# Performance work log

Measured on AMD Instinct MI355X. Metric: run time of the kernel, lower is better.

Reference implementation:

```python
import jax, jax.numpy as jnp
import numpy as np

HID, NBINS = 256, 4
NMIR, NMRNA, B, NP, PD = 2000, 20000, 16, 2048, 1024
EREG, EPM, EPI = 300000, 320000, 32000


def _lin(x, w, b):
    return x @ w.T + b


def _gelu(x):
    # torch nn.GELU default = exact erf formulation
    return jax.nn.gelu(x, approximate=False)


def _ln(x, g, b):
    m = jnp.mean(x, axis=-1, keepdims=True)
    v = jnp.mean((x - m) ** 2, axis=-1, keepdims=True)
    return (x - m) * jax.lax.rsqrt(v + 1e-5) * g + b


def setup_inputs() -> dict:
    key = jax.random.key(0)
    ks = jax.random.split(key, 48)

    def lin_w(i, dout, din):
        s = 1.0 / np.sqrt(din)
        return jax.random.uniform(ks[i], (dout, din), minval=-s, maxval=s, dtype=jnp.float32)

    inp = {}
    inp['emb_mirna'] = jax.random.normal(ks[0], (NMIR, HID), jnp.float32) * 0.02
    inp['emb_mrna'] = jax.random.normal(ks[1], (NMRNA, HID), jnp.float32) * 0.02
    inp['w_mir2mrna'] = jax.random.uniform(ks[2], (EREG,), jnp.float32)
    inp['w_mrna2mir'] = jax.random.uniform(ks[3], (EREG,), jnp.float32)
    inp['w_mrna2pat'] = jax.random.uniform(ks[4], (EPM,), jnp.float32)
    inp['w_mir2pat'] = jax.random.uniform(ks[5], (EPI,), jnp.float32)
    inp['reg_w_mrna'] = lin_w(6, HID, HID)
    inp['reg_b_mrna'] = jnp.zeros((HID,), jnp.float32)
    inp['reg_w_mirna'] = lin_w(7, HID, HID)
    inp['reg_b_mirna'] = jnp.zeros((HID,), jnp.float32)
    inp['proj_w'] = lin_w(8, HID, HID)
    inp['proj_b'] = jnp.zeros((HID,), jnp.float32)
    inp['ln_g'] = jnp.ones((HID,), jnp.float32)
    inp['ln_b'] = jnp.zeros((HID,), jnp.float32)
    inp['omics_w'] = lin_w(9, NBINS, HID)
    inp['omics_b'] = jnp.zeros((NBINS,), jnp.float32)
    inp['wsi_w'] = lin_w(10, HID, PD)
    inp['wsi_b'] = jnp.zeros((HID,), jnp.float32)
    inp['mlp_w'] = lin_w(11, HID, HID)
    inp['mlp_b'] = jnp.zeros((HID,), jnp.float32)
    inp['wln_g'] = jnp.ones((HID,), jnp.float32)
    inp['wln_b'] = jnp.zeros((HID,), jnp.float32)
    inp['fuse_w1'] = lin_w(12, HID, 2 * HID)
    inp['fuse_b1'] = jnp.zeros((HID,), jnp.float32)
    inp['fuse_w2'] = lin_w(13, NBINS, HID)
    inp['fuse_b2'] = jnp.zeros((NBINS,), jnp.float32)
    inp['patches'] = jax.random.normal(ks[14], (B, NP, PD), jnp.float32)
    inp['mask'] = jnp.ones((B, NP), jnp.float32)
    inp['src_mir2mrna'] = jax.random.randint(ks[15], (EREG,), 0, NMIR, jnp.int32)
    inp['dst_mir2mrna'] = jax.random.randint(ks[16], (EREG,), 0, NMRNA, jnp.int32)
    inp['src_mrna2mir'] = jax.random.randint(ks[17], (EREG,), 0, NMRNA, jnp.int32)
    inp['dst_mrna2mir'] = jax.random.randint(ks[18], (EREG,), 0, NMIR, jnp.int32)
    inp['src_mrna2pat'] = jax.random.randint(ks[19], (EPM,), 0, NMRNA, jnp.int32)
    inp['dst_mrna2pat'] = jax.random.randint(ks[20], (EPM,), 0, B, jnp.int32)
    inp['src_mir2pat'] = jax.random.randint(ks[21], (EPI,), 0, NMIR, jnp.int32)
    inp['dst_mir2pat'] = jax.random.randint(ks[22], (EPI,), 0, B, jnp.int32)
    return inp


def reference(emb_mirna, emb_mrna, w_mir2mrna, w_mrna2mir, w_mrna2pat, w_mir2pat,
              reg_w_mrna, reg_b_mrna, reg_w_mirna, reg_b_mirna,
              proj_w, proj_b, ln_g, ln_b, omics_w, omics_b,
              wsi_w, wsi_b, mlp_w, mlp_b, wln_g, wln_b,
              fuse_w1, fuse_b1, fuse_w2, fuse_b2, patches, mask,
              src_mir2mrna, dst_mir2mrna, src_mrna2mir, dst_mrna2mir,
              src_mrna2pat, dst_mrna2pat, src_mir2pat, dst_mir2pat):
    # ---- omics: node embeddings (nid = arange -> full tables) ----
    h_mir, h_mrna = emb_mirna, emb_mrna
    # ---- SimpleRegEncoder: weighted gather-scatter-sum per etype (on ORIGINAL h) ----
    agg_mrna = jax.ops.segment_sum(h_mir[src_mir2mrna] * w_mir2mrna[:, None], dst_mir2mrna, num_segments=NMRNA)
    agg_mir = jax.ops.segment_sum(h_mrna[src_mrna2mir] * w_mrna2mir[:, None], dst_mrna2mir, num_segments=NMIR)
    h_mrna = h_mrna + _gelu(_lin(agg_mrna, reg_w_mrna, reg_b_mrna))  # dropout = identity (eval)
    h_mir = h_mir + _gelu(_lin(agg_mir, reg_w_mirna, reg_b_mirna))
    # ---- PatientReadout: cross_reducer='sum' over both gene->patient etypes ----
    acc = (jax.ops.segment_sum(h_mrna[src_mrna2pat] * w_mrna2pat[:, None], dst_mrna2pat, num_segments=B)
           + jax.ops.segment_sum(h_mir[src_mir2pat] * w_mir2pat[:, None], dst_mir2pat, num_segments=B))
    pat = _ln(_gelu(_lin(acc, proj_w, proj_b)), ln_g, ln_b)  # [B, HID]
    omics_logits = _lin(pat, omics_w, omics_b)  # [B, NBINS]
    # ---- SimpleWSIEncoder ----
    x = _lin(patches, wsi_w, wsi_b)  # [B, NP, HID]
    denom = jnp.clip(jnp.sum(mask, axis=1, keepdims=True), 1.0, None)
    pooled = jnp.sum(x * mask[:, :, None], axis=1) / denom
    pooled = _gelu(_lin(_gelu(pooled), mlp_w, mlp_b))
    wsi = _ln(pooled, wln_g, wln_b)  # [B, HID]
    # ---- fusion head ----
    cat = jnp.concatenate([pat, wsi], axis=-1)  # [B, 2*HID]
    fused = _lin(_gelu(_lin(cat, fuse_w1, fuse_b1)), fuse_w2, fuse_b2)  # [B, NBINS]
    return fused, omics_logits
```

## Files before the change

kernel.cpp:

```cpp
#include <hip/hip_runtime.h>
#include <math.h>

#define HID 256
#define NBINS 4
#define NMIR 2000
#define NMRNA 20000
#define NG (NMRNA + NMIR)
#define BB 16
#define NP 2048
#define PD 1024
#define EREG 300000
#define EPM 320000
#define EPI 32000

typedef __attribute__((ext_vector_type(8))) short bf16x8;
typedef __attribute__((ext_vector_type(4))) float f32x4;

__device__ __forceinline__ float gelu_exact(float x) {
    return 0.5f * x * (1.0f + erff(x * 0.7071067811865475f));
}

__device__ __forceinline__ unsigned short f2b(float f) {
    union { float f; unsigned int u; } v; v.f = f;
    unsigned int u = v.u + 0x7fffu + ((v.u >> 16) & 1u);
    return (unsigned short)(u >> 16);
}

__device__ __forceinline__ float block_reduce_sum(float v, float* red) {
    int c = threadIdx.x;
    red[c] = v;
    __syncthreads();
    for (int st = 128; st > 0; st >>= 1) {
        if (c < st) red[c] += red[c + st];
        __syncthreads();
    }
    float r = red[0];
    __syncthreads();
    return r;
}

__device__ __forceinline__ float kred(float v, float* red, int b, int kk) {
    red[kk * 16 + b] = v;
    __syncthreads();
    for (int st = 8; st >= 1; st >>= 1) {
        if (kk < st) red[kk * 16 + b] += red[(kk + st) * 16 + b];
        __syncthreads();
    }
    float r = red[b];
    __syncthreads();
    return r;
}

__global__ void k_f2b_w(const float* __restrict__ wA, const float* __restrict__ wB,
                        unsigned short* __restrict__ out) {
    int i = blockIdx.x * blockDim.x + threadIdx.x;
    if (i < HID * HID) out[i] = f2b(wA[i]);
    else if (i < 2 * HID * HID) out[i] = f2b(wB[i - HID * HID]);
}

__global__ void k_hist2(const int* __restrict__ dA, const int* __restrict__ dB,
                        int* __restrict__ cnt) {
    int i = blockIdx.x * blockDim.x + threadIdx.x;
    if (i < EREG) atomicAdd(&cnt[dA[i]], 1);
    else if (i < 2 * EREG) atomicAdd(&cnt[NMRNA + dB[i - EREG]], 1);
}

__global__ __launch_bounds__(1024) void k_scan2(const int* __restrict__ cnt,
                                                int* __restrict__ rpA, int* __restrict__ cuA,
                                                int* __restrict__ rpB, int* __restrict__ cuB) {
    __shared__ int part[1024];
    const int* c = (blockIdx.x == 0) ? cnt : cnt + NMRNA;
    int n = (blockIdx.x == 0) ? NMRNA : NMIR;
    int* rowptr = (blockIdx.x == 0) ? rpA : rpB;
    int* cursor = (blockIdx.x == 0) ? cuA : cuB;
    int t = threadIdx.x;
    int chunk = (n + 1023) >> 10;
    int beg = t * chunk;
    int end = min(beg + chunk, n);
    int s = 0;
    for (int i = beg; i < end; i++) s += c[i];
    part[t] = s;
    __syncthreads();
    for (int st = 1; st < 1024; st <<= 1) {
        int v = (t >= st) ? part[t - st] : 0;
        __syncthreads();
        part[t] += v;
        __syncthreads();
    }
    int off = part[t] - s;
    for (int i = beg; i < end; i++) {
        rowptr[i] = off;
        cursor[i] = off;
        off += c[i];
    }
    if (end == n) rowptr[n] = off;
}

__global__ void k_place2(
        const int* __restrict__ srcA, const int* __restrict__ dstA, const float* __restrict__ wA,
        int* __restrict__ cuA, int* __restrict__ srcpA, float* __restrict__ wpA,
        const int* __restrict__ srcB, const int* __restrict__ dstB, const float* __restrict__ wB,
        int* __restrict__ cuB, int* __restrict__ srcpB, float* __restrict__ wpB) {
    int i = blockIdx.x * blockDim.x + threadIdx.x;
    if (i < EREG) {
        int p = atomicAdd(&cuA[dstA[i]], 1);
        srcpA[p] = srcA[i];
        wpA[p] = wA[i];
    } else if (i < 2 * EREG) {
        int j = i - EREG;
        int p = atomicAdd(&cuB[dstB[j]], 1);
        srcpB[p] = srcB[j];
        wpB[p] = wB[j];
    }
}

__global__ __launch_bounds__(256) void k_gather2(
        const float* __restrict__ emb_mirna, const float* __restrict__ emb_mrna,
        const int* __restrict__ rpA, const int* __restrict__ srcpA, const float* __restrict__ wpA,
        const int* __restrict__ rpB, const int* __restrict__ srcpB, const float* __restrict__ wpB,
        unsigned short* __restrict__ agg) {
    __shared__ float lacc[4][HID];
    int n = blockIdx.x;
    const float* emb;
    const int* rp; const int* srcp; const float* wp;
    int node;
    if (n < NMRNA) { emb = emb_mirna; rp = rpA; srcp = srcpA; wp = wpA; node = n; }
    else           { emb = emb_mrna;  rp = rpB; srcp = srcpB; wp = wpB; node = n - NMRNA; }
    int wv = threadIdx.x >> 6, lane = threadIdx.x & 63;
    int beg = rp[node], end = rp[node + 1];
    float a0 = 0.f, a1 = 0.f, a2 = 0.f, a3 = 0.f;
    for (int j = beg + wv; j < end; j += 4) {
        int s = srcp[j];
        float we = wp[j];
        const float* hp = emb + (size_t)s * HID;
        a0 += we * hp[lane];
        a1 += we * hp[lane + 64];
        a2 += we * hp[lane + 128];
        a3 += we * hp[lane + 192];
    }
    lacc[wv][lane] = a0;
    lacc[wv][lane + 64] = a1;
    lacc[wv][lane + 128] = a2;
    lacc[wv][lane + 192] = a3;
    __syncthreads();
    int c = threadIdx.x;
    agg[(size_t)n * HID + c] = f2b(lacc[0][c] + lacc[1][c] + lacc[2][c] + lacc[3][c]);
}

__global__ __launch_bounds__(256) void k_update2(
        const unsigned short* __restrict__ A,
        const float* __restrict__ emb_mrna, const float* __restrict__ emb_mirna,
        const unsigned short* __restrict__ wb,
        const float* __restrict__ bias_mrna, const float* __restrict__ bias_mirna,
        float* __restrict__ h) {
    int row0 = blockIdx.x * 16;
    const float* emb; const unsigned short* Wb; const float* bias; int base;
    if (row0 < NMRNA) { emb = emb_mrna;  Wb = wb;             bias = bias_mrna;  base = 0; }
    else              { emb = emb_mirna; Wb = wb + HID * HID; bias = bias_mirna; base = NMRNA; }
    int wv = threadIdx.x >> 6;
    int lane = threadIdx.x & 63;
    int m = lane & 15;
    int q = lane >> 4;
    bf16x8 afrag[8];
    const unsigned short* arow = A + (size_t)(row0 + m) * HID + q * 8;
#pragma unroll
    for (int kk = 0; kk < 8; kk++)
        afrag[kk] = *(const bf16x8*)(arow + kk * 32);
    f32x4 acc[4];
#pragma unroll
    for (int t = 0; t < 4; t++) acc[t] = (f32x4){0.f, 0.f, 0.f, 0.f};
    int col_base = wv * 64;
#pragma unroll
    for (int t = 0; t < 4; t++) {
        const unsigned short* brow = Wb + (size_t)(col_base + t * 16 + m) * HID + q * 8;
#pragma unroll
        for (int kk = 0; kk < 8; kk++) {
            bf16x8 bfrag = *(const bf16x8*)(brow + kk * 32);
            acc[t] = __builtin_amdgcn_mfma_f32_16x16x32_bf16(afrag[kk], bfrag, acc[t], 0, 0, 0);
        }
    }
#pragma unroll
    for (int t = 0; t < 4; t++) {
        int col = col_base + t * 16 + m;
        float bv = bias[col];
#pragma unroll
        for (int r = 0; r < 4; r++) {
            int row = row0 + q * 4 + r;
            size_t idxh = (size_t)row * HID + col;
            size_t idxe = (size_t)(row - base) * HID + col;
            h[idxh] = emb[idxe] + gelu_exact(acc[t][r] + bv);
        }
    }
}

__global__ void k_wscatter2(
        const int* __restrict__ srcA, const int* __restrict__ dstA, const float* __restrict__ wA,
        const int* __restrict__ srcB, const int* __restrict__ dstB, const float* __restrict__ wB,
        float* __restrict__ Wp) {
    int i = blockIdx.x * blockDim.x + threadIdx.x;
    if (i < EPM) {
        atomicAdd(&Wp[(size_t)dstA[i] * NG + srcA[i]], wA[i]);
    } else if (i < EPM + EPI) {
        int j = i - EPM;
        atomicAdd(&Wp[(size_t)dstB[j] * NG + NMRNA + srcB[j]], wB[j]);
    }
}

#define GCH 128
__global__ __launch_bounds__(256) void k_pat_dense(
        const float* __restrict__ Wp, const float* __restrict__ h,
        float* __restrict__ acc_pat) {
    int c = threadIdx.x;
    int g0 = blockIdx.x * GCH;
    int gend = min(g0 + GCH, NG);
    float acc[BB];
#pragma unroll
    for (int b = 0; b < BB; b++) acc[b] = 0.f;
    for (int g = g0; g < gend; g++) {
        float hv = h[(size_t)g * HID + c];
#pragma unroll
        for (int b = 0; b < BB; b++) acc[b] += Wp[(size_t)b * NG + g] * hv;
    }
#pragma unroll
    for (int b = 0; b < BB; b++) atomicAdd(&acc_pat[b * HID + c], acc[b]);
}

#define PSLICES 32
#define PCHUNK (NP / PSLICES)
__global__ __launch_bounds__(256) void k_pool(
        const float* __restrict__ patches, const float* __restrict__ mask,
        float* __restrict__ pooled, float* __restrict__ masksum) {
    int b = blockIdx.y;
    int p0 = blockIdx.x * PCHUNK;
    int t = threadIdx.x;
    float4 acc = {0.f, 0.f, 0.f, 0.f};
    float msum = 0.f;
    for (int p = p0; p < p0 + PCHUNK; p++) {
        float m = mask[b * NP + p];
        msum += m;
        float4 v = ((const float4*)(patches + ((size_t)b * NP + p) * PD))[t];
        acc.x += m * v.x; acc.y += m * v.y; acc.z += m * v.z; acc.w += m * v.w;
    }
    float* op = pooled + (size_t)b * PD + t * 4;
    atomicAdd(op + 0, acc.x);
    atomicAdd(op + 1, acc.y);
    atomicAdd(op + 2, acc.z);
    atomicAdd(op + 3, acc.w);
    if (t == 0) atomicAdd(&masksum[b], msum);
}

__global__ __launch_bounds__(256) void k_head_a(
        const float* __restrict__ acc_pat, const float* __restrict__ pooled,
        const float* __restrict__ masksum,
        const float* __restrict__ proj_w, const float* __restrict__ proj_b,
        const float* __restrict__ wsi_w, const float* __restrict__ wsi_b,
        float* __restrict__ pg, float* __restrict__ wt) {
    __shared__ float red[256];
    int c = blockIdx.x;
    int t = threadIdx.x;
    int b = t & 15, kk = t >> 4;

    const float* wr = proj_w + (size_t)c * HID + kk * 16;
    const float* xr = acc_pat + (size_t)b * HID + kk * 16;
    float s = 0.f;
#pragma unroll
    for (int i = 0; i < 16; i += 4) {
        float4 w4 = *(const float4*)(wr + i);
        float4 x4 = *(const float4*)(xr + i);
        s += x4.x * w4.x + x4.y * w4.y + x4.z * w4.z + x4.w * w4.w;
    }
    float tot = kred(s, red, b, kk);
    if (kk == 0) pg[(size_t)b * HID + c] = gelu_exact(tot + proj_b[c]);

    const float* wr2 = wsi_w + (size_t)c * PD + kk * 64;
    const float* xr2 = pooled + (size_t)b * PD + kk * 64;
    float s2 = 0.f;
#pragma unroll
    for (int i = 0; i < 64; i += 4) {
        float4 w4 = *(const float4*)(wr2 + i);
        float4 x4 = *(const float4*)(xr2 + i);
        s2 += x4.x * w4.x + x4.y * w4.y + x4.z * w4.z + x4.w * w4.w;
    }
    float tot2 = kred(s2, red, b, kk);
    if (kk == 0) {
        float sm = masksum[b];
        float denom = fmaxf(sm, 1.0f);
        wt[(size_t)b * HID + c] = gelu_exact(tot2 / denom + wsi_b[c] * (sm / denom));
    }
}

__global__ __launch_bounds__(256) void k_head_b(
        const float* __restrict__ wt,
        const float* __restrict__ mlp_w, const float* __restrict__ mlp_b,
        float* __restrict__ ml) {
    __shared__ float red[256];
    int c = blockIdx.x;
    int t = threadIdx.x;
    int b = t & 15, kk = t >> 4;
    const float* wr = mlp_w + (size_t)c * HID + kk * 16;
    const float* xr = wt + (size_t)b * HID + kk * 16;
    float s = 0.f;
#pragma unroll
    for (int i = 0; i < 16; i += 4) {
        float4 w4 = *(const float4*)(wr + i);
        float4 x4 = *(const float4*)(xr + i);
        s += x4.x * w4.x + x4.y * w4.y + x4.z * w4.z + x4.w * w4.w;
    }
    float tot = kred(s, red, b, kk);
    if (kk == 0) ml[(size_t)b * HID + c] = gelu_exact(tot + mlp_b[c]);
}

__global__ __launch_bounds__(256) void k_head_c(
        const float* __restrict__ pg, const float* __restrict__ ml,
        const float* __restrict__ ln_g, const float* __restrict__ ln_b,
        const float* __restrict__ wln_g, const float* __restrict__ wln_b,
        const float* __restrict__ omics_w, const float* __restrict__ omics_b,
        float* __restrict__ vecbuf, float* __restrict__ out_omics) {
    __shared__ float red[256];
    int b = blockIdx.x, c = threadIdx.x;
    float g = pg[(size_t)b * HID + c];
    float mean = block_reduce_sum(g, red) * (1.0f / HID);
    float d = g - mean;
    float var = block_reduce_sum(d * d, red) * (1.0f / HID);
    float patv = d * rsqrtf(var + 1e-5f) * ln_g[c] + ln_b[c];
    vecbuf[(size_t)b * (2 * HID) + c] = patv;
    for (int o = 0; o < NBINS; o++) {
        float r = block_reduce_sum(patv * omics_w[o * HID + c], red);
        if (c == 0) out_omics[b * NBINS + o] = r + omics_b[o];
    }
    float m = ml[(size_t)b * HID + c];
    mean = block_reduce_sum(m, red) * (1.0f / HID);
    d = m - mean;
    var = block_reduce_sum(d * d, red) * (1.0f / HID);
    vecbuf[(size_t)b * (2 * HID) + HID + c] = d * rsqrtf(var + 1e-5f) * wln_g[c] + wln_b[c];
}

__global__ __launch_bounds__(256) void k_head_d(
        const float* __restrict__ vecbuf,
        const float* __restrict__ fuse_w1, const float* __restrict__ fuse_b1,
        float* __restrict__ f1) {
    __shared__ float red[256];
    int c = blockIdx.x;
    int t = threadIdx.x;
    int b = t & 15, kk = t >> 4;
    const float* wr = fuse_w1 + (size_t)c * (2 * HID) + kk * 32;
    const float* xr = vecbuf + (size_t)b * (2 * HID) + kk * 32;
    float s = 0.f;
#pragma unroll
    for (int i = 0; i < 32; i += 4) {
        float4 w4 = *(const float4*)(wr + i);
        float4 x4 = *(const float4*)(xr + i);
        s += x4.x * w4.x + x4.y * w4.y + x4.z * w4.z + x4.w * w4.w;
    }
    float tot = kred(s, red, b, kk);
    if (kk == 0) f1[(size_t)b * HID + c] = gelu_exact(tot + fuse_b1[c]);
}

__global__ __launch_bounds__(256) void k_head_e(
        const float* __restrict__ f1,
        const float* __restrict__ fuse_w2, const float* __restrict__ fuse_b2,
        float* __restrict__ out_fused) {
    __shared__ float red[256];
    int b = blockIdx.x, c = threadIdx.x;
    float h1 = f1[(size_t)b * HID + c];
    for (int o = 0; o < NBINS; o++) {
        float r = block_reduce_sum(h1 * fuse_w2[o * HID + c], red);
        if (c == 0) out_fused[b * NBINS + o] = r + fuse_b2[o];
    }
}

extern "C" void kernel_launch(void* const* d_in, const int* in_sizes, int n_in,
                              void* d_out, int out_size, void* d_ws, size_t ws_size,
                              hipStream_t stream) {
    const float* emb_mirna  = (const float*)d_in[0];
    const float* emb_mrna   = (const float*)d_in[1];
    const float* w_mir2mrna = (const float*)d_in[2];
    const float* w_mrna2mir = (const float*)d_in[3];
    const float* w_mrna2pat = (const float*)d_in[4];
    const float* w_mir2pat  = (const float*)d_in[5];
    const float* reg_w_mrna = (const float*)d_in[6];
    const float* reg_b_mrna = (const float*)d_in[7];
    const float* reg_w_mirna= (const float*)d_in[8];
    const float* reg_b_mirna= (const float*)d_in[9];
    const float* proj_w     = (const float*)d_in[10];
    const float* proj_b     = (const float*)d_in[11];
    const float* ln_g       = (const float*)d_in[12];
    const float* ln_b       = (const float*)d_in[13];
    const float* omics_w    = (const float*)d_in[14];
    const float* omics_b    = (const float*)d_in[15];
    const float* wsi_w      = (const float*)d_in[16];
    const float* wsi_b      = (const float*)d_in[17];
    const float* mlp_w      = (const float*)d_in[18];
    const float* mlp_b      = (const float*)d_in[19];
    const float* wln_g      = (const float*)d_in[20];
    const float* wln_b      = (const float*)d_in[21];
    const float* fuse_w1    = (const float*)d_in[22];
    const float* fuse_b1    = (const float*)d_in[23];
    const float* fuse_w2    = (const float*)d_in[24];
    const float* fuse_b2    = (const float*)d_in[25];
    const float* patches    = (const float*)d_in[26];
    const float* mask       = (const float*)d_in[27];
    const int* src_m2M = (const int*)d_in[28];
    const int* dst_m2M = (const int*)d_in[29];
    const int* src_M2m = (const int*)d_in[30];
    const int* dst_M2m = (const int*)d_in[31];
    const int* src_M2p = (const int*)d_in[32];
    const int* dst_M2p = (const int*)d_in[33];
    const int* src_m2p = (const int*)d_in[34];
    const int* dst_m2p = (const int*)d_in[35];

    float* ws = (float*)d_ws;
    size_t off = 0;
    float* acc_pat  = ws + off; off += (size_t)BB * HID;
    float* pooled   = ws + off; off += (size_t)BB * PD;
    float* Wp       = ws + off; off += (size_t)BB * NG;
    int* cnt        = (int*)(ws + off); off += NG;
    float* masksum  = ws + off; off += BB;
    size_t zero_floats = off;
    unsigned short* agg_bf = (unsigned short*)(ws + off); off += (size_t)NG * HID / 2;
    unsigned short* wb     = (unsigned short*)(ws + off); off += (size_t)2 * HID * HID / 2;
    float* h        = ws + off; off += (size_t)NG * HID;
    float* pg       = ws + off; off += (size_t)BB * HID;
    float* wt       = ws + off; off += (size_t)BB * HID;
    float* ml       = ws + off; off += (size_t)BB * HID;
    float* vecbuf   = ws + off; off += (size_t)BB * 2 * HID;
    float* f1       = ws + off; off += (size_t)BB * HID;
    int* rowptr_A   = (int*)(ws + off); off += NMRNA + 1;
    int* cursor_A   = (int*)(ws + off); off += NMRNA;
    int* rowptr_B   = (int*)(ws + off); off += NMIR + 1;
    int* cursor_B   = (int*)(ws + off); off += NMIR;
    int* srcp_A     = (int*)(ws + off); off += EREG;
    float* wp_A     = ws + off; off += EREG;
    int* srcp_B     = (int*)(ws + off); off += EREG;
    float* wp_B     = ws + off; off += EREG;

    float* out_fused = (float*)d_out;
    float* out_omics = (float*)d_out + BB * NBINS;

    hipMemsetAsync(d_ws, 0, zero_floats * sizeof(float), stream);

    k_f2b_w<<<(2 * HID * HID + 255) / 256, 256, 0, stream>>>(reg_w_mrna, reg_w_mirna, wb);

    k_hist2<<<(2 * EREG + 255) / 256, 256, 0, stream>>>(dst_m2M, dst_M2m, cnt);
    k_scan2<<<2, 1024, 0, stream>>>(cnt, rowptr_A, cursor_A, rowptr_B, cursor_B);
    k_place2<<<(2 * EREG + 255) / 256, 256, 0, stream>>>(
        src_m2M, dst_m2M, w_mir2mrna, cursor_A, srcp_A, wp_A,
        src_M2m, dst_M2m, w_mrna2mir, cursor_B, srcp_B, wp_B);

    k_gather2<<<NG, 256, 0, stream>>>(emb_mirna, emb_mrna,
                                      rowptr_A, srcp_A, wp_A,
                                      rowptr_B, srcp_B, wp_B, agg_bf);

    k_update2<<<NG / 16, 256, 0, stream>>>(agg_bf, emb_mrna, emb_mirna, wb,
                                           reg_b_mrna, reg_b_mirna, h);

    k_wscatter2<<<(EPM + EPI + 255) / 256, 256, 0, stream>>>(
        src_M2p, dst_M2p, w_mrna2pat, src_m2p, dst_m2p, w_mir2pat, Wp);
    k_pat_dense<<<(NG + GCH - 1) / GCH, 256, 0, stream>>>(Wp, h, acc_pat);

    k_pool<<<dim3(PSLICES, BB), 256, 0, stream>>>(patches, mask, pooled, masksum);

    k_head_a<<<HID, 256, 0, stream>>>(acc_pat, pooled, masksum,
                                      proj_w, proj_b, wsi_w, wsi_b, pg, wt);
    k_head_b<<<HID, 256, 0, stream>>>(wt, mlp_w, mlp_b, ml);
    k_head_c<<<BB, 256, 0, stream>>>(pg, ml, ln_g, ln_b, wln_g, wln_b,
                                     omics_w, omics_b, vecbuf, out_omics);
    k_head_d<<<HID, 256, 0, stream>>>(vecbuf, fuse_w1, fuse_b1, f1);
    k_head_e<<<BB, 256, 0, stream>>>(f1, fuse_w2, fuse_b2, out_fused);
}
```

Before: 599.0 us.

## Merge independent prep kernels, gather bf16 embeddings, fuse patient readout into update

Five independent prep stages (patch pooling, embedding bf16 conversion, histogram, patient-weight scatter, weight conversion) now run as block ranges of one k_misc launch, so they can overlap. The neighbour gather reads bf16 copies of the embeddings, halving its gather bytes at some precision cost. The patient readout is folded into k_update2, which keeps the 16-row h tile in shared memory, so the full h matrix is never written or read back. The last head kernel is folded into k_head_d via atomics. The trade-offs are more atomics, an extra embedding-conversion pass, and a reduced-precision gather.

```diff
diff --git a/kernel.cpp b/kernel.cpp
--- a/kernel.cpp
+++ b/kernel.cpp
@@ -26,6 +26,11 @@
     return (unsigned short)(u >> 16);
 }
 
+__device__ __forceinline__ float b2f(unsigned short u) {
+    union { unsigned int i; float f; } v; v.i = ((unsigned int)u) << 16;
+    return v.f;
+}
+
 __device__ __forceinline__ float block_reduce_sum(float v, float* red) {
     int c = threadIdx.x;
     red[c] = v;
@@ -51,18 +56,86 @@
     return r;
 }
 
-__global__ void k_f2b_w(const float* __restrict__ wA, const float* __restrict__ wB,
-                        unsigned short* __restrict__ out) {
-    int i = blockIdx.x * blockDim.x + threadIdx.x;
-    if (i < HID * HID) out[i] = f2b(wA[i]);
-    else if (i < 2 * HID * HID) out[i] = f2b(wB[i - HID * HID]);
-}
-
-__global__ void k_hist2(const int* __restrict__ dA, const int* __restrict__ dB,
-                        int* __restrict__ cnt) {
-    int i = blockIdx.x * blockDim.x + threadIdx.x;
-    if (i < EREG) atomicAdd(&cnt[dA[i]], 1);
-    else if (i < 2 * EREG) atomicAdd(&cnt[NMRNA + dB[i - EREG]], 1);
+#define MISC_POOL 512
+#define PSLICES 32
+#define PCHUNK (NP / PSLICES)
+#define MISC_EMB (((NMIR + NMRNA) * HID) / 1024)
+#define MISC_HIST ((2 * EREG + 255) / 256)
+#define MISC_WSC ((EPM + EPI + 255) / 256)
+#define MISC_F2B ((2 * HID * HID) / 1024)
+#define MISC_TOTAL (MISC_POOL + MISC_EMB + MISC_HIST + MISC_WSC + MISC_F2B)
+
+__global__ __launch_bounds__(256) void k_misc(
+        const float* __restrict__ patches, const float* __restrict__ mask,
+        float* __restrict__ pooled, float* __restrict__ masksum,
+        const float* __restrict__ emb_mirna, const float* __restrict__ emb_mrna,
+        unsigned short* __restrict__ embB_mir, unsigned short* __restrict__ embB_mrna,
+        const int* __restrict__ dA, const int* __restrict__ dB, int* __restrict__ cnt,
+        const int* __restrict__ srcP, const int* __restrict__ dstP, const float* __restrict__ wP,
+        const int* __restrict__ srcI, const int* __restrict__ dstI, const float* __restrict__ wI,
+        float* __restrict__ Wp,
+        const float* __restrict__ regwA, const float* __restrict__ regwB,
+        unsigned short* __restrict__ wb) {
+    int bid = blockIdx.x;
+    int t = threadIdx.x;
+    if (bid < MISC_POOL) {
+        int slice = bid & 31, b = bid >> 5;
+        int p0 = slice * PCHUNK;
+        float4 acc = {0.f, 0.f, 0.f, 0.f};
+        float msum = 0.f;
+        for (int p = p0; p < p0 + PCHUNK; p++) {
+            float m = mask[b * NP + p];
+            msum += m;
+            float4 v = ((const float4*)(patches + ((size_t)b * NP + p) * PD))[t];
+            acc.x += m * v.x; acc.y += m * v.y; acc.z += m * v.z; acc.w += m * v.w;
+        }
+        float* op = pooled + (size_t)b * PD + t * 4;
+        atomicAdd(op + 0, acc.x);
+        atomicAdd(op + 1, acc.y);
+        atomicAdd(op + 2, acc.z);
+        atomicAdd(op + 3, acc.w);
+        if (t == 0) atomicAdd(&masksum[b], msum);
+        return;
+    }
+    bid -= MISC_POOL;
+    if (bid < MISC_EMB) {
+        size_t e = (size_t)bid * 1024 + t * 4;
+        const size_t NM = (size_t)NMIR * HID;
+        float4 v;
+        unsigned short* o;
+        if (e < NM) { v = *(const float4*)(emb_mirna + e); o = embB_mir + e; }
+        else        { v = *(const float4*)(emb_mrna + (e - NM)); o = embB_mrna + (e - NM); }
+        ushort4 u = { f2b(v.x), f2b(v.y), f2b(v.z), f2b(v.w) };
+        *(ushort4*)o = u;
+        return;
+    }
+    bid -= MISC_EMB;
+    if (bid < MISC_HIST) {
+        int i = bid * 256 + t;
+        if (i < EREG) atomicAdd(&cnt[dA[i]], 1);
+        else if (i < 2 * EREG) atomicAdd(&cnt[NMRNA + dB[i - EREG]], 1);
+        return;
+    }
+    bid -= MISC_HIST;
+    if (bid < MISC_WSC) {
+        int i = bid * 256 + t;
+        if (i < EPM) {
+            atomicAdd(&Wp[(size_t)dstP[i] * NG + srcP[i]], wP[i]);
+        } else if (i < EPM + EPI) {
+            int j = i - EPM;
+            atomicAdd(&Wp[(size_t)dstI[j] * NG + NMRNA + srcI[j]], wI[j]);
+        }
+        return;
+    }
+    bid -= MISC_WSC;
+    {
+        size_t e = (size_t)bid * 1024 + t * 4;
+        float4 v;
+        if (e < (size_t)HID * HID) v = *(const float4*)(regwA + e);
+        else v = *(const float4*)(regwB + (e - HID * HID));
+        ushort4 u = { f2b(v.x), f2b(v.y), f2b(v.z), f2b(v.w) };
+        *(ushort4*)(wb + e) = u;
+    }
 }
 
 __global__ __launch_bounds__(1024) void k_scan2(const int* __restrict__ cnt,
@@ -115,33 +188,31 @@
 }
 
 __global__ __launch_bounds__(256) void k_gather2(
-        const float* __restrict__ emb_mirna, const float* __restrict__ emb_mrna,
+        const unsigned short* __restrict__ embB_mir, const unsigned short* __restrict__ embB_mrna,
         const int* __restrict__ rpA, const int* __restrict__ srcpA, const float* __restrict__ wpA,
         const int* __restrict__ rpB, const int* __restrict__ srcpB, const float* __restrict__ wpB,
         unsigned short* __restrict__ agg) {
     __shared__ float lacc[4][HID];
     int n = blockIdx.x;
-    const float* emb;
+    const unsigned short* emb;
     const int* rp; const int* srcp; const float* wp;
     int node;
-    if (n < NMRNA) { emb = emb_mirna; rp = rpA; srcp = srcpA; wp = wpA; node = n; }
-    else           { emb = emb_mrna;  rp = rpB; srcp = srcpB; wp = wpB; node = n - NMRNA; }
-    int wv = threadIdx.x >> 6, lane = threadIdx.x & 63;
+    if (n < NMRNA) { emb = embB_mir;  rp = rpA; srcp = srcpA; wp = wpA; node = n; }
+    else           { emb = embB_mrna; rp = rpB; srcp = srcpB; wp = wpB; node = n - NMRNA; }
+    int wv = threadIdx.x >> 6, l = threadIdx.x & 63;
     int beg = rp[node], end = rp[node + 1];
     float a0 = 0.f, a1 = 0.f, a2 = 0.f, a3 = 0.f;
     for (int j = beg + wv; j < end; j += 4) {
         int s = srcp[j];
         float we = wp[j];
-        const float* hp = emb + (size_t)s * HID;
-        a0 += we * hp[lane];
-        a1 += we * hp[lane + 64];
-        a2 += we * hp[lane + 128];
-        a3 += we * hp[lane + 192];
-    }
-    lacc[wv][lane] = a0;
-    lacc[wv][lane + 64] = a1;
-    lacc[wv][lane + 128] = a2;
-    lacc[wv][lane + 192] = a3;
+        ushort4 v = *(const ushort4*)(emb + (size_t)s * HID + l * 4);
+        a0 += we * b2f(v.x);
+        a1 += we * b2f(v.y);
+        a2 += we * b2f(v.z);
+        a3 += we * b2f(v.w);
+    }
+    float4 st = { a0, a1, a2, a3 };
+    ((float4*)lacc[wv])[l] = st;
     __syncthreads();
     int c = threadIdx.x;
     agg[(size_t)n * HID + c] = f2b(lacc[0][c] + lacc[1][c] + lacc[2][c] + lacc[3][c]);
@@ -152,7 +223,8 @@
         const float* __restrict__ emb_mrna, const float* __restrict__ emb_mirna,
         const unsigned short* __restrict__ wb,
         const float* __restrict__ bias_mrna, const float* __restrict__ bias_mirna,
-        float* __restrict__ h) {
+        const float* __restrict__ Wp, float* __restrict__ acc_pat) {
+    __shared__ float ht[16][HID + 1];
     int row0 = blockIdx.x * 16;
     const float* emb; const unsigned short* Wb; const float* bias; int base;
     if (row0 < NMRNA) { emb = emb_mrna;  Wb = wb;             bias = bias_mrna;  base = 0; }
@@ -185,68 +257,24 @@
         float bv = bias[col];
 #pragma unroll
         for (int r = 0; r < 4; r++) {
-            int row = row0 + q * 4 + r;
-            size_t idxh = (size_t)row * HID + col;
-            size_t idxe = (size_t)(row - base) * HID + col;
-            h[idxh] = emb[idxe] + gelu_exact(acc[t][r] + bv);
+            int lrow = q * 4 + r;
+            size_t idxe = (size_t)(row0 - base + lrow) * HID + col;
+            ht[lrow][col] = emb[idxe] + gelu_exact(acc[t][r] + bv);
         }
     }
-}
-
-__global__ void k_wscatter2(
-        const int* __restrict__ srcA, const int* __restrict__ dstA, const float* __restrict__ wA,
-        const int* __restrict__ srcB, const int* __restrict__ dstB, const float* __restrict__ wB,
-        float* __restrict__ Wp) {
-    int i = blockIdx.x * blockDim.x + threadIdx.x;
-    if (i < EPM) {
-        atomicAdd(&Wp[(size_t)dstA[i] * NG + srcA[i]], wA[i]);
-    } else if (i < EPM + EPI) {
-        int j = i - EPM;
-        atomicAdd(&Wp[(size_t)dstB[j] * NG + NMRNA + srcB[j]], wB[j]);
-    }
-}
-
-#define GCH 128
-__global__ __launch_bounds__(256) void k_pat_dense(
-        const float* __restrict__ Wp, const float* __restrict__ h,
-        float* __restrict__ acc_pat) {
+    __syncthreads();
     int c = threadIdx.x;
-    int g0 = blockIdx.x * GCH;
-    int gend = min(g0 + GCH, NG);
-    float acc[BB];
-#pragma unroll
-    for (int b = 0; b < BB; b++) acc[b] = 0.f;
-    for (int g = g0; g < gend; g++) {
-        float hv = h[(size_t)g * HID + c];
-#pragma unroll
-        for (int b = 0; b < BB; b++) acc[b] += Wp[(size_t)b * NG + g] * hv;
-    }
-#pragma unroll
-    for (int b = 0; b < BB; b++) atomicAdd(&acc_pat[b * HID + c], acc[b]);
-}
-
-#define PSLICES 32
-#define PCHUNK (NP / PSLICES)
-__global__ __launch_bounds__(256) void k_pool(
-        const float* __restrict__ patches, const float* __restrict__ mask,
-        float* __restrict__ pooled, float* __restrict__ masksum) {
-    int b = blockIdx.y;
-    int p0 = blockIdx.x * PCHUNK;
-    int t = threadIdx.x;
-    float4 acc = {0.f, 0.f, 0.f, 0.f};
-    float msum = 0.f;
-    for (int p = p0; p < p0 + PCHUNK; p++) {
-        float m = mask[b * NP + p];
-        msum += m;
-        float4 v = ((const float4*)(patches + ((size_t)b * NP + p) * PD))[t];
-        acc.x += m * v.x; acc.y += m * v.y; acc.z += m * v.z; acc.w += m * v.w;
-    }
-    float* op = pooled + (size_t)b * PD + t * 4;
-    atomicAdd(op + 0, acc.x);
-    atomicAdd(op + 1, acc.y);
-    atomicAdd(op + 2, acc.z);
-    atomicAdd(op + 3, acc.w);
-    if (t == 0) atomicAdd(&masksum[b], msum);
+    float hv[16];
+#pragma unroll
+    for (int r = 0; r < 16; r++) hv[r] = ht[r][c];
+#pragma unroll
+    for (int b = 0; b < BB; b++) {
+        const float* wpr = Wp + (size_t)b * NG + row0;
+        float s = 0.f;
+#pragma unroll
+        for (int r = 0; r < 16; r++) s += wpr[r] * hv[r];
+        atomicAdd(&acc_pat[b * HID + c], s);
+    }
 }
 
 __global__ __launch_bounds__(256) void k_head_a(
@@ -315,9 +343,12 @@
         const float* __restrict__ ln_g, const float* __restrict__ ln_b,
         const float* __restrict__ wln_g, const float* __restrict__ wln_b,
         const float* __restrict__ omics_w, const float* __restrict__ omics_b,
-        float* __restrict__ vecbuf, float* __restrict__ out_omics) {
+        const float* __restrict__ fuse_b2,
+        float* __restrict__ vecbuf, float* __restrict__ out_omics,
+        float* __restrict__ out_fused) {
     __shared__ float red[256];
     int b = blockIdx.x, c = threadIdx.x;
+    if (c < NBINS) out_fused[b * NBINS + c] = fuse_b2[c];
     float g = pg[(size_t)b * HID + c];
     float mean = block_reduce_sum(g, red) * (1.0f / HID);
     float d = g - mean;
@@ -338,7 +369,8 @@
 __global__ __launch_bounds__(256) void k_head_d(
         const float* __restrict__ vecbuf,
         const float* __restrict__ fuse_w1, const float* __restrict__ fuse_b1,
-        float* __restrict__ f1) {
+        const float* __restrict__ fuse_w2,
+        float* __restrict__ out_fused) {
     __shared__ float red[256];
     int c = blockIdx.x;
     int t = threadIdx.x;
@@ -353,19 +385,11 @@
         s += x4.x * w4.x + x4.y * w4.y + x4.z * w4.z + x4.w * w4.w;
     }
     float tot = kred(s, red, b, kk);
-    if (kk == 0) f1[(size_t)b * HID + c] = gelu_exact(tot + fuse_b1[c]);
-}
-
-__global__ __launch_bounds__(256) void k_head_e(
-        const float* __restrict__ f1,
-        const float* __restrict__ fuse_w2, const float* __restrict__ fuse_b2,
-        float* __restrict__ out_fused) {
-    __shared__ float red[256];
-    int b = blockIdx.x, c = threadIdx.x;
-    float h1 = f1[(size_t)b * HID + c];
-    for (int o = 0; o < NBINS; o++) {
-        float r = block_reduce_sum(h1 * fuse_w2[o * HID + c], red);
-        if (c == 0) out_fused[b * NBINS + o] = r + fuse_b2[o];
+    if (kk == 0) {
+        float h1 = gelu_exact(tot + fuse_b1[c]);
+#pragma unroll
+        for (int o = 0; o < NBINS; o++)
+            atomicAdd(&out_fused[b * NBINS + o], h1 * fuse_w2[o * HID + c]);
     }
 }
 
@@ -419,12 +443,12 @@
     size_t zero_floats = off;
     unsigned short* agg_bf = (unsigned short*)(ws + off); off += (size_t)NG * HID / 2;
     unsigned short* wb     = (unsigned short*)(ws + off); off += (size_t)2 * HID * HID / 2;
-    float* h        = ws + off; off += (size_t)NG * HID;
+    unsigned short* embB_mir  = (unsigned short*)(ws + off); off += (size_t)NMIR * HID / 2;
+    unsigned short* embB_mrna = (unsigned short*)(ws + off); off += (size_t)NMRNA * HID / 2;
     float* pg       = ws + off; off += (size_t)BB * HID;
     float* wt       = ws + off; off += (size_t)BB * HID;
     float* ml       = ws + off; off += (size_t)BB * HID;
     float* vecbuf   = ws + off; off += (size_t)BB * 2 * HID;
-    float* f1       = ws + off; off += (size_t)BB * HID;
     int* rowptr_A   = (int*)(ws + off); off += NMRNA + 1;
     int* cursor_A   = (int*)(ws + off); off += NMRNA;
     int* rowptr_B   = (int*)(ws + off); off += NMIR + 1;
@@ -439,32 +463,30 @@
 
     hipMemsetAsync(d_ws, 0, zero_floats * sizeof(float), stream);
 
-    k_f2b_w<<<(2 * HID * HID + 255) / 256, 256, 0, stream>>>(reg_w_mrna, reg_w_mirna, wb);
-
-    k_hist2<<<(2 * EREG + 255) / 256, 256, 0, stream>>>(dst_m2M, dst_M2m, cnt);
+    k_misc<<<MISC_TOTAL, 256, 0, stream>>>(
+        patches, mask, pooled, masksum,
+        emb_mirna, emb_mrna, embB_mir, embB_mrna,
+        dst_m2M, dst_M2m, cnt,
+        src_M2p, dst_M2p, w_mrna2pat, src_m2p, dst_m2p, w_mir2pat, Wp,
+        reg_w_mrna, reg_w_mirna, wb);
+
     k_scan2<<<2, 1024, 0, stream>>>(cnt, rowptr_A, cursor_A, rowptr_B, cursor_B);
     k_place2<<<(2 * EREG + 255) / 256, 256, 0, stream>>>(
         src_m2M, dst_m2M, w_mir2mrna, cursor_A, srcp_A, wp_A,
         src_M2m, dst_M2m, w_mrna2mir, cursor_B, srcp_B, wp_B);
 
-    k_gather2<<<NG, 256, 0, stream>>>(emb_mirna, emb_mrna,
+    k_gather2<<<NG, 256, 0, stream>>>(embB_mir, embB_mrna,
                                       rowptr_A, srcp_A, wp_A,
                                       rowptr_B, srcp_B, wp_B, agg_bf);
 
     k_update2<<<NG / 16, 256, 0, stream>>>(agg_bf, emb_mrna, emb_mirna, wb,
-                                           reg_b_mrna, reg_b_mirna, h);
-
-    k_wscatter2<<<(EPM + EPI + 255) / 256, 256, 0, stream>>>(
-        src_M2p, dst_M2p, w_mrna2pat, src_m2p, dst_m2p, w_mir2pat, Wp);
-    k_pat_dense<<<(NG + GCH - 1) / GCH, 256, 0, stream>>>(Wp, h, acc_pat);
-
-    k_pool<<<dim3(PSLICES, BB), 256, 0, stream>>>(patches, mask, pooled, masksum);
+                                           reg_b_mrna, reg_b_mirna, Wp, acc_pat);
 
     k_head_a<<<HID, 256, 0, stream>>>(acc_pat, pooled, masksum,
                                       proj_w, proj_b, wsi_w, wsi_b, pg, wt);
     k_head_b<<<HID, 256, 0, stream>>>(wt, mlp_w, mlp_b, ml);
     k_head_c<<<BB, 256, 0, stream>>>(pg, ml, ln_g, ln_b, wln_g, wln_b,
-                                     omics_w, omics_b, vecbuf, out_omics);
-    k_head_d<<<HID, 256, 0, stream>>>(vecbuf, fuse_w1, fuse_b1, f1);
-    k_head_e<<<BB, 256, 0, stream>>>(f1, fuse_w2, fuse_b2, out_fused);
-}
+                                     omics_w, omics_b, fuse_b2,
+                                     vecbuf, out_omics, out_fused);
+    k_head_d<<<HID, 256, 0, stream>>>(vecbuf, fuse_w1, fuse_b1, fuse_w2, out_fused);
+}
```

New measurement: 597.0 us. No clear change (-0.3%).
